# Kernel tuning notes

Measured on AMD Instinct MI355X. Metric: run time of the kernel, lower is better.

The kernel has to match this reference:

```python
import jax, jax.numpy as jnp
import numpy as np

EMBEDDING_DIM = 64

def setup_inputs() -> dict:
    key = jax.random.key(0)
    kq, kk, kv = jax.random.split(key, 3)
    shape = (8, 8, 2048, 64)  # [B, H, S, D]
    return {
        "query": jax.random.normal(kq, shape, dtype=jnp.float32),
        "key": jax.random.normal(kk, shape, dtype=jnp.float32),
        "value": jax.random.normal(kv, shape, dtype=jnp.float32),
    }

def reference(query, key, value):
    # dot_product = Q @ K^T over last two dims
    scores = jnp.einsum('bhqd,bhkd->bhqk', query, key)
    # Faithful to source: scaler = d**0.5, then divide by sqrt(scaler) => d**0.25
    scale = jnp.sqrt(jnp.asarray(EMBEDDING_DIM ** 0.5, dtype=scores.dtype))
    attn = jax.nn.softmax(scores / scale, axis=-1)
    return jnp.einsum('bhqk,bhkd->bhqd', attn, value)
```

## Files before the change

### kernel.cpp

```cpp
#include <hip/hip_runtime.h>

typedef _Float16 f16;
typedef _Float16 half8 __attribute__((ext_vector_type(8)));
typedef __fp16 h2 __attribute__((ext_vector_type(2)));
typedef float f32x16 __attribute__((ext_vector_type(16)));
typedef unsigned int u32x2 __attribute__((ext_vector_type(2)));

constexpr int S  = 2048;
constexpr int D  = 64;
constexpr int TQ = 128;
constexpr int TK = 64;
constexpr int KP = 72;
constexpr int VP = 72;
constexpr int TP = 66;
constexpr int HEADS = 64;
constexpr size_t HSZ = (size_t)S * D;
constexpr size_t KG_BYTES = (size_t)HEADS * HSZ * 2;
constexpr float MSUB = 14.0f;

__global__ __launch_bounds__(256) void prep(const float* __restrict__ K,
                                            const float* __restrict__ V,
                                            f16* __restrict__ Kg,
                                            f16* __restrict__ Vt) {
    __shared__ __align__(16) f16 Ts[64 * TP];
    const int t = threadIdx.x;
    const size_t hb = (size_t)blockIdx.y * HSZ;
    const int k0 = blockIdx.x * 64;
    const int row = t >> 2, c = (t & 3) * 16;

    {
        const float* src = K + hb + (size_t)(k0 + row) * D + c;
        f16* dst = Kg + hb + (size_t)(k0 + row) * D + c;
        #pragma unroll
        for (int u = 0; u < 2; ++u) {
            float4 a = *(const float4*)(src + u * 8);
            float4 b = *(const float4*)(src + u * 8 + 4);
            half8 h;
            h[0] = (f16)a.x; h[1] = (f16)a.y; h[2] = (f16)a.z; h[3] = (f16)a.w;
            h[4] = (f16)b.x; h[5] = (f16)b.y; h[6] = (f16)b.z; h[7] = (f16)b.w;
            *(half8*)(dst + u * 8) = h;
        }
    }
    {
        const float* src = V + hb + (size_t)(k0 + row) * D + c;
        f16* dst = &Ts[row * TP + c];
        #pragma unroll
        for (int u = 0; u < 4; ++u) {
            float4 a = *(const float4*)(src + u * 4);
            *(h2*)(dst + u * 4)     = __builtin_amdgcn_cvt_pkrtz(a.x, a.y);
            *(h2*)(dst + u * 4 + 2) = __builtin_amdgcn_cvt_pkrtz(a.z, a.w);
        }
    }
    __syncthreads();
    {
        const int d = row, kc = c;
        f16 tmp[16];
        #pragma unroll
        for (int i = 0; i < 16; ++i) tmp[i] = Ts[(kc + i) * TP + d];
        f16* dst = Vt + hb + (size_t)d * S + k0 + kc;
        *(half8*)dst       = *(half8*)&tmp[0];
        *(half8*)(dst + 8) = *(half8*)&tmp[8];
    }
}

__device__ __forceinline__ u32x2 plswap(unsigned int a, unsigned int b) {
#if __has_builtin(__builtin_amdgcn_permlane32_swap)
    return __builtin_amdgcn_permlane32_swap(a, b, false, false);
#else
    asm volatile("v_permlane32_swap_b32 %0, %1" : "+v"(a), "+v"(b));
    u32x2 r; r[0] = a; r[1] = b; return r;
#endif
}

__device__ __forceinline__ void sm_pack(f32x16 z, float& l_part, half8* pa2) {
    #pragma unroll
    for (int r = 0; r < 16; ++r) z[r] = __builtin_amdgcn_exp2f(z[r]);
    {
        float a0 = z[0] + z[1],   a1 = z[2] + z[3];
        float a2 = z[4] + z[5],   a3 = z[6] + z[7];
        float a4 = z[8] + z[9],   a5 = z[10] + z[11];
        float a6 = z[12] + z[13], a7 = z[14] + z[15];
        l_part += ((a0 + a1) + (a2 + a3)) + ((a4 + a5) + (a6 + a7));
    }
    unsigned int W[8];
    #pragma unroll
    for (int j = 0; j < 8; ++j) {
        union { h2 h; unsigned int u; } c;
        c.h = __builtin_amdgcn_cvt_pkrtz(z[2 * j], z[2 * j + 1]);
        W[j] = c.u;
    }
    #pragma unroll
    for (int kbl = 0; kbl < 2; ++kbl) {
        u32x2 sa = plswap(W[4 * kbl + 0], W[4 * kbl + 2]);
        u32x2 sb = plswap(W[4 * kbl + 1], W[4 * kbl + 3]);
        union { unsigned int u[4]; half8 h; } t;
        t.u[0] = sa[0]; t.u[1] = sb[0]; t.u[2] = sa[1]; t.u[3] = sb[1];
        pa2[kbl] = t.h;
    }
}

__global__ __launch_bounds__(256, 4) void attn_fwd(
    const float* __restrict__ Q, const f16* __restrict__ Kg,
    const f16* __restrict__ Vt, float* __restrict__ O)
{
    __shared__ __align__(16) f16 Ks[2][TK * KP];
    __shared__ __align__(16) f16 Vs[2][D * VP];
    __shared__ float linv[128];

    const int tid  = threadIdx.x;
    const int w    = tid >> 6;
    const int lane = tid & 63;
    const int l31  = lane & 31;
    const int hi   = lane >> 5;

    const int lid  = blockIdx.y * 16 + blockIdx.x;
    const int phys = (lid & 7) * 128 + (lid >> 3);
    const int head = phys >> 4;
    const int qb   = phys & 15;
    const size_t hb = (size_t)head * HSZ;
    const int qbase = qb * TQ + w * 32;

    const float SCALE = 0.35355339059327373f * 1.44269504088896340f;

    half8 qf[4];
    #pragma unroll
    for (int db = 0; db < 4; ++db) {
        const float* qp = Q + hb + (size_t)(qbase + l31) * D + db * 16 + hi * 8;
        float4 a = *(const float4*)(qp);
        float4 b = *(const float4*)(qp + 4);
        half8 h;
        h[0] = (f16)(a.x * SCALE); h[1] = (f16)(a.y * SCALE);
        h[2] = (f16)(a.z * SCALE); h[3] = (f16)(a.w * SCALE);
        h[4] = (f16)(b.x * SCALE); h[5] = (f16)(b.y * SCALE);
        h[6] = (f16)(b.z * SCALE); h[7] = (f16)(b.w * SCALE);
        qf[db] = h;
    }

    f32x16 accO[2];
    #pragma unroll
    for (int r = 0; r < 16; ++r) { accO[0][r] = 0.0f; accO[1][r] = 0.0f; }
    float l_part = 0.0f;

    const int srow = tid >> 2, sc = (tid & 3) * 16;
    const f16* Kg0 = Kg + hb + (size_t)srow * D + sc;
    const f16* Vg0 = Vt + hb + (size_t)srow * S + sc;
    f16* ksd0 = &Ks[0][srow * KP + sc];
    f16* vsd0 = &Vs[0][srow * VP + sc];
    f16* ksd1 = &Ks[1][srow * KP + sc];
    f16* vsd1 = &Vs[1][srow * VP + sc];

    constexpr int NT = S / TK;
    half8 kA = *(const half8*)Kg0, kB = *(const half8*)(Kg0 + 8);
    half8 vA = *(const half8*)Vg0, vB = *(const half8*)(Vg0 + 8);

    for (int kt = 0; kt < NT; ++kt) {
        const int p = kt & 1;
        {
            f16* ksd = p ? ksd1 : ksd0;
            f16* vsd = p ? vsd1 : vsd0;
            *(half8*)ksd = kA; *(half8*)(ksd + 8) = kB;
            *(half8*)vsd = vA; *(half8*)(vsd + 8) = vB;
        }
        __syncthreads();

        if (kt + 1 < NT) {
            const f16* kp = Kg0 + (size_t)(kt + 1) * TK * D;
            const f16* vp = Vg0 + (size_t)(kt + 1) * TK;
            kA = *(const half8*)kp; kB = *(const half8*)(kp + 8);
            vA = *(const half8*)vp; vB = *(const half8*)(vp + 8);
        }

        half8 pa[4];

        f32x16 z;
        #pragma unroll
        for (int r = 0; r < 16; ++r) z[r] = -MSUB;
        #pragma unroll
        for (int db = 0; db < 4; ++db) {
            half8 kf = *(const half8*)&Ks[p][l31 * KP + db * 16 + hi * 8];
            z = __builtin_amdgcn_mfma_f32_32x32x16_f16(kf, qf[db], z, 0, 0, 0);
        }
        sm_pack(z, l_part, &pa[0]);

        f32x16 z2;
        #pragma unroll
        for (int r = 0; r < 16; ++r) z2[r] = -MSUB;
        #pragma unroll
        for (int db = 0; db < 4; ++db) {
            half8 kf = *(const half8*)&Ks[p][(32 + l31) * KP + db * 16 + hi * 8];
            z2 = __builtin_amdgcn_mfma_f32_32x32x16_f16(kf, qf[db], z2, 0, 0, 0);
        }

        #pragma unroll
        for (int nt = 0; nt < 2; ++nt)
            #pragma unroll
            for (int kb = 0; kb < 2; ++kb) {
                half8 vf = *(const half8*)&Vs[p][(nt * 32 + l31) * VP + kb * 16 + hi * 8];
                accO[nt] = __builtin_amdgcn_mfma_f32_32x32x16_f16(pa[kb], vf, accO[nt], 0, 0, 0);
            }

        sm_pack(z2, l_part, &pa[2]);

        #pragma unroll
        for (int nt = 0; nt < 2; ++nt)
            #pragma unroll
            for (int kb = 2; kb < 4; ++kb) {
                half8 vf = *(const half8*)&Vs[p][(nt * 32 + l31) * VP + kb * 16 + hi * 8];
                accO[nt] = __builtin_amdgcn_mfma_f32_32x32x16_f16(pa[kb], vf, accO[nt], 0, 0, 0);
            }
    }

    float l = l_part + __shfl_xor(l_part, 32);
    linv[w * 32 + l31] = 1.0f / l;
    __syncthreads();

    #pragma unroll
    for (int nt = 0; nt < 2; ++nt)
        #pragma unroll
        for (int r = 0; r < 16; ++r) {
            const int qrow = (r & 3) + 8 * (r >> 2) + 4 * hi;
            const float iv = linv[w * 32 + qrow];
            O[hb + (size_t)(qbase + qrow) * D + nt * 32 + l31] = accO[nt][r] * iv;
        }
}

extern "C" void kernel_launch(void* const* d_in, const int* in_sizes, int n_in,
                              void* d_out, int out_size, void* d_ws, size_t ws_size,
                              hipStream_t stream) {
    const float* q = (const float*)d_in[0];
    const float* k = (const float*)d_in[1];
    const float* v = (const float*)d_in[2];
    float* o = (float*)d_out;
    f16* Kg = (f16*)d_ws;
    f16* Vg = (f16*)((char*)d_ws + KG_BYTES);

    prep<<<dim3(S / 64, HEADS), 256, 0, stream>>>(k, v, Kg, Vg);
    attn_fwd<<<dim3(S / TQ, HEADS), 256, 0, stream>>>(q, Kg, Vg, o);
}
```

Baseline: 205.1 us.

## Process two 32-row query groups per wave to reuse K/V fragments

Each wave now handles 64 query rows instead of 32, so the block tile grows to 256 queries. Every K and V fragment read from LDS feeds two MFMA chains, which halves LDS traffic and global K/V loads per query, and the interleaved independent chains give the scheduler more work to hide latency. The cost is roughly doubled accumulator and Q register use, hence launch bounds drop to 2 blocks per SM. The grid also halves to 512 blocks, which risks lower occupancy and poorer load balance across CUs.

```diff
diff --git a/kernel.cpp b/kernel.cpp
--- a/kernel.cpp
+++ b/kernel.cpp
@@ -8,7 +8,7 @@
 
 constexpr int S  = 2048;
 constexpr int D  = 64;
-constexpr int TQ = 128;
+constexpr int TQ = 256;
 constexpr int TK = 64;
 constexpr int KP = 72;
 constexpr int VP = 72;
@@ -99,13 +99,13 @@
     }
 }
 
-__global__ __launch_bounds__(256, 4) void attn_fwd(
+__global__ __launch_bounds__(256, 2) void attn_fwd(
     const float* __restrict__ Q, const f16* __restrict__ Kg,
     const f16* __restrict__ Vt, float* __restrict__ O)
 {
     __shared__ __align__(16) f16 Ks[2][TK * KP];
     __shared__ __align__(16) f16 Vs[2][D * VP];
-    __shared__ float linv[128];
+    __shared__ float linv[256];
 
     const int tid  = threadIdx.x;
     const int w    = tid >> 6;
@@ -113,33 +113,43 @@
     const int l31  = lane & 31;
     const int hi   = lane >> 5;
 
-    const int lid  = blockIdx.y * 16 + blockIdx.x;
-    const int phys = (lid & 7) * 128 + (lid >> 3);
-    const int head = phys >> 4;
-    const int qb   = phys & 15;
+    const int lid  = blockIdx.y * (S / TQ) + blockIdx.x;
+    const int phys = (lid & 7) * 64 + (lid >> 3);
+    const int head = phys >> 3;
+    const int qb   = phys & 7;
     const size_t hb = (size_t)head * HSZ;
-    const int qbase = qb * TQ + w * 32;
+    const int qbase = qb * TQ + w * 64;
 
     const float SCALE = 0.35355339059327373f * 1.44269504088896340f;
 
-    half8 qf[4];
-    #pragma unroll
-    for (int db = 0; db < 4; ++db) {
-        const float* qp = Q + hb + (size_t)(qbase + l31) * D + db * 16 + hi * 8;
-        float4 a = *(const float4*)(qp);
-        float4 b = *(const float4*)(qp + 4);
-        half8 h;
-        h[0] = (f16)(a.x * SCALE); h[1] = (f16)(a.y * SCALE);
-        h[2] = (f16)(a.z * SCALE); h[3] = (f16)(a.w * SCALE);
-        h[4] = (f16)(b.x * SCALE); h[5] = (f16)(b.y * SCALE);
-        h[6] = (f16)(b.z * SCALE); h[7] = (f16)(b.w * SCALE);
-        qf[db] = h;
-    }
-
-    f32x16 accO[2];
-    #pragma unroll
-    for (int r = 0; r < 16; ++r) { accO[0][r] = 0.0f; accO[1][r] = 0.0f; }
-    float l_part = 0.0f;
+    half8 qf[2][4];
+    #pragma unroll
+    for (int g = 0; g < 2; ++g)
+        #pragma unroll
+        for (int db = 0; db < 4; ++db) {
+            const float* qp = Q + hb + (size_t)(qbase + g * 32 + l31) * D + db * 16 + hi * 8;
+            float4 a = *(const float4*)(qp);
+            float4 b = *(const float4*)(qp + 4);
+            half8 h;
+            h[0] = (f16)(a.x * SCALE); h[1] = (f16)(a.y * SCALE);
+            h[2] = (f16)(a.z * SCALE); h[3] = (f16)(a.w * SCALE);
+            h[4] = (f16)(b.x * SCALE); h[5] = (f16)(b.y * SCALE);
+            h[6] = (f16)(b.z * SCALE); h[7] = (f16)(b.w * SCALE);
+            qf[g][db] = h;
+        }
+
+    f32x16 minit;
+    #pragma unroll
+    for (int r = 0; r < 16; ++r) minit[r] = -MSUB;
+
+    f32x16 accO[2][2];
+    #pragma unroll
+    for (int g = 0; g < 2; ++g)
+        #pragma unroll
+        for (int nt = 0; nt < 2; ++nt)
+            #pragma unroll
+            for (int r = 0; r < 16; ++r) accO[g][nt][r] = 0.0f;
+    float l0 = 0.0f, l1 = 0.0f;
 
     const int srow = tid >> 2, sc = (tid & 3) * 16;
     const f16* Kg0 = Kg + hb + (size_t)srow * D + sc;
@@ -170,58 +180,81 @@
             vA = *(const half8*)vp; vB = *(const half8*)(vp + 8);
         }
 
-        half8 pa[4];
-
-        f32x16 z;
-        #pragma unroll
-        for (int r = 0; r < 16; ++r) z[r] = -MSUB;
-        #pragma unroll
-        for (int db = 0; db < 4; ++db) {
-            half8 kf = *(const half8*)&Ks[p][l31 * KP + db * 16 + hi * 8];
-            z = __builtin_amdgcn_mfma_f32_32x32x16_f16(kf, qf[db], z, 0, 0, 0);
-        }
-        sm_pack(z, l_part, &pa[0]);
-
-        f32x16 z2;
-        #pragma unroll
-        for (int r = 0; r < 16; ++r) z2[r] = -MSUB;
-        #pragma unroll
-        for (int db = 0; db < 4; ++db) {
-            half8 kf = *(const half8*)&Ks[p][(32 + l31) * KP + db * 16 + hi * 8];
-            z2 = __builtin_amdgcn_mfma_f32_32x32x16_f16(kf, qf[db], z2, 0, 0, 0);
-        }
+        half8 pa0[4], pa1[4];
+        f32x16 z00, z10, z01, z11;
+
+        {
+            half8 kf0 = *(const half8*)&Ks[p][l31 * KP +  0 + hi * 8];
+            half8 kf1 = *(const half8*)&Ks[p][l31 * KP + 16 + hi * 8];
+            half8 kf2 = *(const half8*)&Ks[p][l31 * KP + 32 + hi * 8];
+            half8 kf3 = *(const half8*)&Ks[p][l31 * KP + 48 + hi * 8];
+            z00 = __builtin_amdgcn_mfma_f32_32x32x16_f16(kf0, qf[0][0], minit, 0, 0, 0);
+            z00 = __builtin_amdgcn_mfma_f32_32x32x16_f16(kf1, qf[0][1], z00, 0, 0, 0);
+            z00 = __builtin_amdgcn_mfma_f32_32x32x16_f16(kf2, qf[0][2], z00, 0, 0, 0);
+            z00 = __builtin_amdgcn_mfma_f32_32x32x16_f16(kf3, qf[0][3], z00, 0, 0, 0);
+            z10 = __builtin_amdgcn_mfma_f32_32x32x16_f16(kf0, qf[1][0], minit, 0, 0, 0);
+            z10 = __builtin_amdgcn_mfma_f32_32x32x16_f16(kf1, qf[1][1], z10, 0, 0, 0);
+            z10 = __builtin_amdgcn_mfma_f32_32x32x16_f16(kf2, qf[1][2], z10, 0, 0, 0);
+            z10 = __builtin_amdgcn_mfma_f32_32x32x16_f16(kf3, qf[1][3], z10, 0, 0, 0);
+        }
+        sm_pack(z00, l0, &pa0[0]);
+
+        {
+            half8 kf0 = *(const half8*)&Ks[p][(32 + l31) * KP +  0 + hi * 8];
+            half8 kf1 = *(const half8*)&Ks[p][(32 + l31) * KP + 16 + hi * 8];
+            half8 kf2 = *(const half8*)&Ks[p][(32 + l31) * KP + 32 + hi * 8];
+            half8 kf3 = *(const half8*)&Ks[p][(32 + l31) * KP + 48 + hi * 8];
+            z01 = __builtin_amdgcn_mfma_f32_32x32x16_f16(kf0, qf[0][0], minit, 0, 0, 0);
+            z01 = __builtin_amdgcn_mfma_f32_32x32x16_f16(kf1, qf[0][1], z01, 0, 0, 0);
+            z01 = __builtin_amdgcn_mfma_f32_32x32x16_f16(kf2, qf[0][2], z01, 0, 0, 0);
+            z01 = __builtin_amdgcn_mfma_f32_32x32x16_f16(kf3, qf[0][3], z01, 0, 0, 0);
+            z11 = __builtin_amdgcn_mfma_f32_32x32x16_f16(kf0, qf[1][0], minit, 0, 0, 0);
+            z11 = __builtin_amdgcn_mfma_f32_32x32x16_f16(kf1, qf[1][1], z11, 0, 0, 0);
+            z11 = __builtin_amdgcn_mfma_f32_32x32x16_f16(kf2, qf[1][2], z11, 0, 0, 0);
+            z11 = __builtin_amdgcn_mfma_f32_32x32x16_f16(kf3, qf[1][3], z11, 0, 0, 0);
+        }
+        sm_pack(z10, l1, &pa1[0]);
 
         #pragma unroll
         for (int nt = 0; nt < 2; ++nt)
             #pragma unroll
             for (int kb = 0; kb < 2; ++kb) {
                 half8 vf = *(const half8*)&Vs[p][(nt * 32 + l31) * VP + kb * 16 + hi * 8];
-                accO[nt] = __builtin_amdgcn_mfma_f32_32x32x16_f16(pa[kb], vf, accO[nt], 0, 0, 0);
+                accO[0][nt] = __builtin_amdgcn_mfma_f32_32x32x16_f16(pa0[kb], vf, accO[0][nt], 0, 0, 0);
+                accO[1][nt] = __builtin_amdgcn_mfma_f32_32x32x16_f16(pa1[kb], vf, accO[1][nt], 0, 0, 0);
             }
 
-        sm_pack(z2, l_part, &pa[2]);
+        sm_pack(z01, l0, &pa0[2]);
+        sm_pack(z11, l1, &pa1[2]);
 
         #pragma unroll
         for (int nt = 0; nt < 2; ++nt)
             #pragma unroll
             for (int kb = 2; kb < 4; ++kb) {
                 half8 vf = *(const half8*)&Vs[p][(nt * 32 + l31) * VP + kb * 16 + hi * 8];
-                accO[nt] = __builtin_amdgcn_mfma_f32_32x32x16_f16(pa[kb], vf, accO[nt], 0, 0, 0);
+                accO[0][nt] = __builtin_amdgcn_mfma_f32_32x32x16_f16(pa0[kb], vf, accO[0][nt], 0, 0, 0);
+                accO[1][nt] = __builtin_amdgcn_mfma_f32_32x32x16_f16(pa1[kb], vf, accO[1][nt], 0, 0, 0);
             }
     }
 
-    float l = l_part + __shfl_xor(l_part, 32);
-    linv[w * 32 + l31] = 1.0f / l;
+    {
+        float t0 = l0 + __shfl_xor(l0, 32);
+        float t1 = l1 + __shfl_xor(l1, 32);
+        linv[w * 64 + l31]      = 1.0f / t0;
+        linv[w * 64 + 32 + l31] = 1.0f / t1;
+    }
     __syncthreads();
 
     #pragma unroll
-    for (int nt = 0; nt < 2; ++nt)
-        #pragma unroll
-        for (int r = 0; r < 16; ++r) {
-            const int qrow = (r & 3) + 8 * (r >> 2) + 4 * hi;
-            const float iv = linv[w * 32 + qrow];
-            O[hb + (size_t)(qbase + qrow) * D + nt * 32 + l31] = accO[nt][r] * iv;
-        }
+    for (int g = 0; g < 2; ++g)
+        #pragma unroll
+        for (int nt = 0; nt < 2; ++nt)
+            #pragma unroll
+            for (int r = 0; r < 16; ++r) {
+                const int qrow = (r & 3) + 8 * (r >> 2) + 4 * hi;
+                const float iv = linv[w * 64 + g * 32 + qrow];
+                O[hb + (size_t)(qbase + g * 32 + qrow) * D + nt * 32 + l31] = accO[g][nt][r] * iv;
+            }
 }
 
 extern "C" void kernel_launch(void* const* d_in, const int* in_sizes, int n_in,
```

Measured after the change: 201.6 us. No clear change (-1.7%).

## Software-pipeline QK^T of next tile with softmax and PV of current tile

Applied to the files above, without the earlier changes.

Restructures the attention loop so the QK^T MFMAs for tile kt+1 are issued before the exp/pack and PV MFMAs for tile kt. Both K and V shared buffers are double-buffered with a rotating schedule, and the loop is unrolled by two. The goal is to overlap matrix-core work with the VALU softmax work. In exchange it adds a second barrier per iteration, does a redundant QK on the last iteration, and lowers the launch-bounds occupancy hint from 4 to 2 to make room for extra live accumulators, which may reduce latency hiding across waves.

```diff
diff --git a/kernel.cpp b/kernel.cpp
--- a/kernel.cpp
+++ b/kernel.cpp
@@ -99,7 +99,7 @@
     }
 }
 
-__global__ __launch_bounds__(256, 4) void attn_fwd(
+__global__ __launch_bounds__(256, 2) void attn_fwd(
     const float* __restrict__ Q, const f16* __restrict__ Kg,
     const f16* __restrict__ Vt, float* __restrict__ O)
 {
@@ -136,6 +136,10 @@
         qf[db] = h;
     }
 
+    f32x16 minit;
+    #pragma unroll
+    for (int r = 0; r < 16; ++r) minit[r] = -MSUB;
+
     f32x16 accO[2];
     #pragma unroll
     for (int r = 0; r < 16; ++r) { accO[0][r] = 0.0f; accO[1][r] = 0.0f; }
@@ -150,64 +154,82 @@
     f16* vsd1 = &Vs[1][srow * VP + sc];
 
     constexpr int NT = S / TK;
-    half8 kA = *(const half8*)Kg0, kB = *(const half8*)(Kg0 + 8);
-    half8 vA = *(const half8*)Vg0, vB = *(const half8*)(Vg0 + 8);
-
-    for (int kt = 0; kt < NT; ++kt) {
-        const int p = kt & 1;
+    half8 kA, kB, vA, vB;
+
+    auto qk = [&](const f16* ksbuf, f32x16& o0, f32x16& o1) {
         {
-            f16* ksd = p ? ksd1 : ksd0;
-            f16* vsd = p ? vsd1 : vsd0;
-            *(half8*)ksd = kA; *(half8*)(ksd + 8) = kB;
-            *(half8*)vsd = vA; *(half8*)(vsd + 8) = vB;
-        }
+            half8 kf0 = *(const half8*)&ksbuf[l31 * KP +  0 + hi * 8];
+            half8 kf1 = *(const half8*)&ksbuf[l31 * KP + 16 + hi * 8];
+            half8 kf2 = *(const half8*)&ksbuf[l31 * KP + 32 + hi * 8];
+            half8 kf3 = *(const half8*)&ksbuf[l31 * KP + 48 + hi * 8];
+            o0 = __builtin_amdgcn_mfma_f32_32x32x16_f16(kf0, qf[0], minit, 0, 0, 0);
+            o0 = __builtin_amdgcn_mfma_f32_32x32x16_f16(kf1, qf[1], o0, 0, 0, 0);
+            o0 = __builtin_amdgcn_mfma_f32_32x32x16_f16(kf2, qf[2], o0, 0, 0, 0);
+            o0 = __builtin_amdgcn_mfma_f32_32x32x16_f16(kf3, qf[3], o0, 0, 0, 0);
+        }
+        {
+            half8 kf0 = *(const half8*)&ksbuf[(32 + l31) * KP +  0 + hi * 8];
+            half8 kf1 = *(const half8*)&ksbuf[(32 + l31) * KP + 16 + hi * 8];
+            half8 kf2 = *(const half8*)&ksbuf[(32 + l31) * KP + 32 + hi * 8];
+            half8 kf3 = *(const half8*)&ksbuf[(32 + l31) * KP + 48 + hi * 8];
+            o1 = __builtin_amdgcn_mfma_f32_32x32x16_f16(kf0, qf[0], minit, 0, 0, 0);
+            o1 = __builtin_amdgcn_mfma_f32_32x32x16_f16(kf1, qf[1], o1, 0, 0, 0);
+            o1 = __builtin_amdgcn_mfma_f32_32x32x16_f16(kf2, qf[2], o1, 0, 0, 0);
+            o1 = __builtin_amdgcn_mfma_f32_32x32x16_f16(kf3, qf[3], o1, 0, 0, 0);
+        }
+    };
+
+    {
+        kA = *(const half8*)Kg0; kB = *(const half8*)(Kg0 + 8);
+        vA = *(const half8*)Vg0; vB = *(const half8*)(Vg0 + 8);
+        *(half8*)ksd0 = kA; *(half8*)(ksd0 + 8) = kB;
+        *(half8*)vsd0 = vA; *(half8*)(vsd0 + 8) = vB;
+    }
+    __syncthreads();
+    {
+        const f16* kp = Kg0 + (size_t)TK * D;
+        const f16* vp = Vg0 + (size_t)TK;
+        kA = *(const half8*)kp; kB = *(const half8*)(kp + 8);
+        vA = *(const half8*)vp; vB = *(const half8*)(vp + 8);
+    }
+    f32x16 zA0, zA1, zB0, zB1;
+    qk(&Ks[0][0], zA0, zA1);
+
+    auto body = [&](int kt, f16* ksN, f16* vsN, const f16* KsN, const f16* VsC,
+                    f32x16& zc0, f32x16& zc1, f32x16& zn0, f32x16& zn1) {
+        *(half8*)ksN = kA; *(half8*)(ksN + 8) = kB;
+        *(half8*)vsN = vA; *(half8*)(vsN + 8) = vB;
         __syncthreads();
 
-        if (kt + 1 < NT) {
-            const f16* kp = Kg0 + (size_t)(kt + 1) * TK * D;
-            const f16* vp = Vg0 + (size_t)(kt + 1) * TK;
+        {
+            const int nxt = (kt + 2 < NT) ? (kt + 2) : (NT - 1);
+            const f16* kp = Kg0 + (size_t)nxt * TK * D;
+            const f16* vp = Vg0 + (size_t)nxt * TK;
             kA = *(const half8*)kp; kB = *(const half8*)(kp + 8);
             vA = *(const half8*)vp; vB = *(const half8*)(vp + 8);
         }
 
+        qk(KsN, zn0, zn1);
+
         half8 pa[4];
-
-        f32x16 z;
-        #pragma unroll
-        for (int r = 0; r < 16; ++r) z[r] = -MSUB;
-        #pragma unroll
-        for (int db = 0; db < 4; ++db) {
-            half8 kf = *(const half8*)&Ks[p][l31 * KP + db * 16 + hi * 8];
-            z = __builtin_amdgcn_mfma_f32_32x32x16_f16(kf, qf[db], z, 0, 0, 0);
-        }
-        sm_pack(z, l_part, &pa[0]);
-
-        f32x16 z2;
-        #pragma unroll
-        for (int r = 0; r < 16; ++r) z2[r] = -MSUB;
-        #pragma unroll
-        for (int db = 0; db < 4; ++db) {
-            half8 kf = *(const half8*)&Ks[p][(32 + l31) * KP + db * 16 + hi * 8];
-            z2 = __builtin_amdgcn_mfma_f32_32x32x16_f16(kf, qf[db], z2, 0, 0, 0);
-        }
+        sm_pack(zc0, l_part, &pa[0]);
+        sm_pack(zc1, l_part, &pa[2]);
 
         #pragma unroll
         for (int nt = 0; nt < 2; ++nt)
             #pragma unroll
-            for (int kb = 0; kb < 2; ++kb) {
-                half8 vf = *(const half8*)&Vs[p][(nt * 32 + l31) * VP + kb * 16 + hi * 8];
+            for (int kb = 0; kb < 4; ++kb) {
+                half8 vf = *(const half8*)&VsC[(nt * 32 + l31) * VP + kb * 16 + hi * 8];
                 accO[nt] = __builtin_amdgcn_mfma_f32_32x32x16_f16(pa[kb], vf, accO[nt], 0, 0, 0);
             }
 
-        sm_pack(z2, l_part, &pa[2]);
-
-        #pragma unroll
-        for (int nt = 0; nt < 2; ++nt)
-            #pragma unroll
-            for (int kb = 2; kb < 4; ++kb) {
-                half8 vf = *(const half8*)&Vs[p][(nt * 32 + l31) * VP + kb * 16 + hi * 8];
-                accO[nt] = __builtin_amdgcn_mfma_f32_32x32x16_f16(pa[kb], vf, accO[nt], 0, 0, 0);
-            }
+        asm volatile("s_waitcnt lgkmcnt(0)" ::: "memory");
+        __builtin_amdgcn_s_barrier();
+    };
+
+    for (int kt2 = 0; kt2 < NT; kt2 += 2) {
+        body(kt2,     ksd1, vsd1, &Ks[1][0], &Vs[0][0], zA0, zA1, zB0, zB1);
+        body(kt2 + 1, ksd0, vsd0, &Ks[0][0], &Vs[1][0], zB0, zB1, zA0, zA1);
     }
 
     float l = l_part + __shfl_xor(l_part, 32);
```

After: 207.4 us. No clear change (+1.1%).
